# Optimization experiments

Hardware: AMD Instinct MI355X
Metric: run time of the kernel (lower is better)

The kernel has to match this reference:

```python
import jax, jax.numpy as jnp
import numpy as np

N_SP = 1024          # number of superpixels per image (max index + 1)
FEATURE_DIM = 256
HIDDEN_DIM = 128
OUTPUT_DIM = 64
TEMPERATURE = 0.1
B, H, W = 4, 256, 256


def setup_inputs() -> dict:
    key = jax.random.key(0)
    ks = jax.random.split(key, 12)
    features = jax.random.normal(ks[0], (B, FEATURE_DIM, H, W), dtype=jnp.float32)
    superpixel_indices = jax.random.randint(ks[1], (B, H, W), 0, N_SP, dtype=jnp.int32)
    s = 0.02
    return {
        "features": features,
        "superpixel_indices": superpixel_indices,
        "W1": jax.random.normal(ks[2], (HIDDEN_DIM, FEATURE_DIM), jnp.float32) * s,
        "b1": jnp.zeros((HIDDEN_DIM,), jnp.float32),
        "W2": jax.random.normal(ks[3], (HIDDEN_DIM, HIDDEN_DIM), jnp.float32) * s,
        "b2": jnp.zeros((HIDDEN_DIM,), jnp.float32),
        "Wp1": jax.random.normal(ks[4], (OUTPUT_DIM, HIDDEN_DIM), jnp.float32) * s,
        "bp1": jnp.zeros((OUTPUT_DIM,), jnp.float32),
        "Wp2": jax.random.normal(ks[5], (OUTPUT_DIM, HIDDEN_DIM), jnp.float32) * s,
        "bp2": jnp.zeros((OUTPUT_DIM,), jnp.float32),
    }


def _aggregate(feat, idx):
    # feat: [C,H,W], idx: [H,W] -> scatter-mean into [N_SP, C]
    C = feat.shape[0]
    feat_flat = feat.reshape(C, -1).T           # [HW, C]
    idx_flat = idx.reshape(-1)
    seg_sum = jax.ops.segment_sum(feat_flat, idx_flat, num_segments=N_SP)
    counts = jax.ops.segment_sum(jnp.ones_like(idx_flat, dtype=feat.dtype), idx_flat,
                                 num_segments=N_SP)[:, None]  # [N_SP,1]
    sp_feat = jnp.where(counts > 0, seg_sum / jnp.maximum(counts, 1.0), 0.0)
    return sp_feat


def _adjacency(idx):
    # idx: [H,W] int -> symmetric normalized adjacency [N_SP, N_SP]
    s1 = jnp.concatenate([idx[:, :-1].reshape(-1), idx[:-1, :].reshape(-1)])
    s2 = jnp.concatenate([idx[:, 1:].reshape(-1), idx[1:, :].reshape(-1)])
    diff = (s1 != s2).astype(jnp.float32)
    adj = jnp.zeros((N_SP, N_SP), jnp.float32).at[s1, s2].add(diff)
    adj = ((adj + adj.T) > 0).astype(jnp.float32) + jnp.eye(N_SP, dtype=jnp.float32)
    deg = jnp.sqrt(adj.sum(axis=1))
    adj = adj / (deg[:, None] * deg[None, :])
    return adj


def _infonce(z1, z2):
    z1 = z1 / jnp.linalg.norm(z1, axis=1, keepdims=True)
    z2 = z2 / jnp.linalg.norm(z2, axis=1, keepdims=True)
    sim = (z1 @ z2.T) / TEMPERATURE            # [N,N]
    loss = -jnp.diagonal(sim) + jax.scipy.special.logsumexp(sim, axis=1)
    return loss.mean()


def reference(features, superpixel_indices, W1, b1, W2, b2, Wp1, bp1, Wp2, bp2):
    def per_image(feat, idx):
        sp_feat = _aggregate(feat, idx)        # [N_SP, C]
        adj = _adjacency(idx)                  # [N_SP, N_SP]
        x = adj @ sp_feat                      # graph conv
        h = jax.nn.relu(x @ W1.T + b1)         # encoder (dropout = identity, eval)
        h = jax.nn.relu(h @ W2.T + b2)
        z1 = h @ Wp1.T + bp1
        z2 = h @ Wp2.T + bp2
        return _infonce(z1, z2)
    losses = jax.vmap(per_image)(features, superpixel_indices)
    return losses.mean()
```

## Files before the change

kernel.cpp:

```cpp
#include <hip/hip_runtime.h>
#include <math.h>

#define NB 4
#define NC 256
#define NPIX 65536
#define NSP 1024
#define OUTD 64

typedef short bfrag_t __attribute__((ext_vector_type(8)));
typedef float cfrag_t __attribute__((ext_vector_type(4)));
typedef float f32x2 __attribute__((ext_vector_type(2)));

__device__ __forceinline__ unsigned short f2bf(float f) {
    union { float f; unsigned u; } v; v.f = f;
    unsigned r = (v.u + 0x7FFFu + ((v.u >> 16) & 1u)) >> 16;
    return (unsigned short)r;
}
__device__ __forceinline__ float bf2f(unsigned short h) {
    union { unsigned u; float f; } v; v.u = ((unsigned)h) << 16;
    return v.f;
}

__global__ __launch_bounds__(256) void hist_kernel(const int* __restrict__ idx,
                                                   unsigned* __restrict__ counts_u) {
    __shared__ unsigned cnt[NSP];
    int b = blockIdx.y;
    int tid = threadIdx.x;
    for (int s = tid; s < NSP; s += 256) cnt[s] = 0u;
    __syncthreads();
    const int4* idx4 = (const int4*)(idx + b * NPIX + blockIdx.x * 1024);
    int4 s4 = idx4[tid];
    atomicAdd(&cnt[s4.x], 1u);
    atomicAdd(&cnt[s4.y], 1u);
    atomicAdd(&cnt[s4.z], 1u);
    atomicAdd(&cnt[s4.w], 1u);
    __syncthreads();
    for (int s = tid; s < NSP; s += 256)
        if (cnt[s]) atomicAdd(&counts_u[b * NSP + s], cnt[s]);
}

__global__ __launch_bounds__(256) void scan_kernel(const unsigned* __restrict__ counts_u,
                                                   unsigned* __restrict__ offsets,
                                                   unsigned* __restrict__ cursor) {
    int b = blockIdx.x;
    int tid = threadIdx.x;
    __shared__ unsigned v[256];
    unsigned c0 = counts_u[b * NSP + tid * 4 + 0];
    unsigned c1 = counts_u[b * NSP + tid * 4 + 1];
    unsigned c2 = counts_u[b * NSP + tid * 4 + 2];
    unsigned c3 = counts_u[b * NSP + tid * 4 + 3];
    v[tid] = c0 + c1 + c2 + c3;
    __syncthreads();
    for (int off = 1; off < 256; off <<= 1) {
        unsigned t = (tid >= off) ? v[tid - off] : 0u;
        __syncthreads();
        v[tid] += t;
        __syncthreads();
    }
    unsigned base = tid ? v[tid - 1] : 0u;
    unsigned o0 = base, o1 = base + c0, o2 = base + c0 + c1, o3 = base + c0 + c1 + c2;
    offsets[b * (NSP + 1) + tid * 4 + 0] = o0;
    offsets[b * (NSP + 1) + tid * 4 + 1] = o1;
    offsets[b * (NSP + 1) + tid * 4 + 2] = o2;
    offsets[b * (NSP + 1) + tid * 4 + 3] = o3;
    cursor[b * NSP + tid * 4 + 0] = o0;
    cursor[b * NSP + tid * 4 + 1] = o1;
    cursor[b * NSP + tid * 4 + 2] = o2;
    cursor[b * NSP + tid * 4 + 3] = o3;
    if (tid == 255) offsets[b * (NSP + 1) + NSP] = v[255];
}

__global__ __launch_bounds__(256) void rank_kernel(const int* __restrict__ idx,
                                                   unsigned* __restrict__ cursor,
                                                   int* __restrict__ rank) {
    __shared__ unsigned lcnt[NSP];
    __shared__ unsigned base[NSP];
    int b = blockIdx.y;
    int tid = threadIdx.x;
    for (int s = tid; s < NSP; s += 256) lcnt[s] = 0u;
    __syncthreads();
    const int4* idx4 = (const int4*)(idx + b * NPIX + blockIdx.x * 1024);
    int4 s4 = idx4[tid];
    unsigned r0 = atomicAdd(&lcnt[s4.x], 1u);
    unsigned r1 = atomicAdd(&lcnt[s4.y], 1u);
    unsigned r2 = atomicAdd(&lcnt[s4.z], 1u);
    unsigned r3 = atomicAdd(&lcnt[s4.w], 1u);
    __syncthreads();
    for (int s = tid; s < NSP; s += 256) {
        unsigned c = lcnt[s];
        base[s] = c ? atomicAdd(&cursor[b * NSP + s], c) : 0u;
    }
    __syncthreads();
    int p = b * NPIX + blockIdx.x * 1024 + tid * 4;
    rank[p + 0] = (int)(base[s4.x] + r0);
    rank[p + 1] = (int)(base[s4.y] + r1);
    rank[p + 2] = (int)(base[s4.z] + r2);
    rank[p + 3] = (int)(base[s4.w] + r3);
}

__global__ __launch_bounds__(256) void transpose_kernel(const float* __restrict__ feat,
                                                        const int* __restrict__ rank,
                                                        unsigned char* __restrict__ featP) {
    __shared__ unsigned short tile[64 * 260];
    __shared__ int rk[64];
    int b = blockIdx.y;
    int p0 = blockIdx.x * 64;
    int tid = threadIdx.x;
    if (tid < 64) rk[tid] = rank[b * NPIX + p0 + tid];
    int cg = tid >> 4;
    int x4 = tid & 15;
    #pragma unroll
    for (int pass = 0; pass < 16; ++pass) {
        int c = pass * 16 + cg;
        float4 v = *(const float4*)&feat[((size_t)(b * NC + c)) * NPIX + p0 + x4 * 4];
        tile[(x4 * 4 + 0) * 260 + c] = f2bf(v.x);
        tile[(x4 * 4 + 1) * 260 + c] = f2bf(v.y);
        tile[(x4 * 4 + 2) * 260 + c] = f2bf(v.z);
        tile[(x4 * 4 + 3) * 260 + c] = f2bf(v.w);
    }
    __syncthreads();
    int c4 = tid & 63;
    int r0 = tid >> 6;
    #pragma unroll
    for (int pass = 0; pass < 16; ++pass) {
        int row = pass * 4 + r0;
        ushort4 w = *(const ushort4*)&tile[row * 260 + c4 * 4];
        float f0 = bf2f(w.x), f1 = bf2f(w.y), f2 = bf2f(w.z), f3 = bf2f(w.w);
        int lo = __builtin_amdgcn_cvt_pk_fp8_f32(f0, f1, 0, false);
        int pk = __builtin_amdgcn_cvt_pk_fp8_f32(f2, f3, lo, true);
        *(unsigned*)&featP[((size_t)b * NPIX + rk[row]) * NC + c4 * 4] = (unsigned)pk;
    }
}

__global__ __launch_bounds__(256) void segsum_kernel(const unsigned char* __restrict__ featP,
                                                     const unsigned* __restrict__ offsets,
                                                     const float* __restrict__ deg_inv,
                                                     float* __restrict__ spf) {
    __shared__ float red[4][256];
    int b = blockIdx.y, s = blockIdx.x;
    int tid = threadIdx.x;
    int w = tid >> 6, lane = tid & 63;
    unsigned j0 = offsets[b * (NSP + 1) + s];
    unsigned j1 = offsets[b * (NSP + 1) + s + 1];
    const unsigned* base = (const unsigned*)(featP + (size_t)b * NPIX * NC);
    float a0 = 0.f, a1 = 0.f, a2 = 0.f, a3 = 0.f;
    for (unsigned j = j0 + w; j < j1; j += 4) {
        unsigned u = base[(size_t)j * 64 + lane];
        f32x2 lo = __builtin_amdgcn_cvt_pk_f32_fp8(u, false);
        f32x2 hi = __builtin_amdgcn_cvt_pk_f32_fp8(u, true);
        a0 += lo.x; a1 += lo.y; a2 += hi.x; a3 += hi.y;
    }
    *(float4*)&red[w][lane * 4] = (float4){a0, a1, a2, a3};
    __syncthreads();
    int c = tid;
    float sum = red[0][c] + red[1][c] + red[2][c] + red[3][c];
    unsigned cnt = j1 - j0;
    float scale = cnt ? deg_inv[b * NSP + s] / (float)cnt : 0.f;
    spf[((size_t)b * NSP + s) * NC + c] = sum * scale;
}

__global__ __launch_bounds__(256) void spft_kernel(const float* __restrict__ spf,
                                                   unsigned short* __restrict__ spfT) {
    __shared__ unsigned short t[64 * 68];
    int b = blockIdx.z;
    int s0 = blockIdx.x * 64, c0 = blockIdx.y * 64;
    int tid = threadIdx.x;
    int sl = tid >> 4, c4 = tid & 15;
    #pragma unroll
    for (int it = 0; it < 4; ++it) {
        int s = it * 16 + sl;
        float4 v = *(const float4*)&spf[((size_t)b * NSP + s0 + s) * NC + c0 + c4 * 4];
        t[(c4 * 4 + 0) * 68 + s] = f2bf(v.x);
        t[(c4 * 4 + 1) * 68 + s] = f2bf(v.y);
        t[(c4 * 4 + 2) * 68 + s] = f2bf(v.z);
        t[(c4 * 4 + 3) * 68 + s] = f2bf(v.w);
    }
    __syncthreads();
    int cl = tid >> 4, s4 = tid & 15;
    #pragma unroll
    for (int it = 0; it < 4; ++it) {
        int c = it * 16 + cl;
        ushort4 w = *(const ushort4*)&t[c * 68 + s4 * 4];
        *(ushort4*)&spfT[((size_t)b * NC + c0 + c) * NSP + s0 + s4 * 4] = w;
    }
}

__global__ __launch_bounds__(256) void adj_kernel(const int* __restrict__ idx,
                                                  unsigned short* __restrict__ adj) {
    const int PAIRS = 65280;
    const int PERB = 2 * PAIRS + NSP;
    int i = blockIdx.x * 256 + threadIdx.x;
    if (i >= NB * PERB) return;
    int b = i / PERB;
    int r = i % PERB;
    unsigned short* A = adj + (size_t)b * NSP * NSP;
    const int* id = idx + b * NPIX;
    if (r >= 2 * PAIRS) {
        int s = r - 2 * PAIRS;
        A[s * NSP + s] = 0x3F80;
        return;
    }
    int p1, p2;
    if (r < PAIRS) {
        int row = r / 255, col = r % 255;
        p1 = row * 256 + col; p2 = p1 + 1;
    } else {
        int rv = r - PAIRS;
        p1 = rv; p2 = rv + 256;
    }
    int s1 = id[p1], s2 = id[p2];
    if (s1 != s2) {
        A[s1 * NSP + s2] = 0x3F80;
        A[s2 * NSP + s1] = 0x3F80;
    }
}

__global__ __launch_bounds__(256) void deg_kernel(const unsigned short* __restrict__ adj,
                                                  float* __restrict__ deg_inv) {
    int row = blockIdx.x;
    int tid = threadIdx.x;
    const unsigned* a2 = (const unsigned*)(adj + (size_t)row * NSP);
    unsigned u0 = a2[tid], u1 = a2[tid + 256];
    float s = (float)((u0 & 0xFFFFu) != 0) + (float)((u0 >> 16) != 0)
            + (float)((u1 & 0xFFFFu) != 0) + (float)((u1 >> 16) != 0);
    for (int off = 32; off > 0; off >>= 1) s += __shfl_down(s, off, 64);
    __shared__ float wsum[4];
    if ((tid & 63) == 0) wsum[tid >> 6] = s;
    __syncthreads();
    if (tid == 0) deg_inv[row] = 1.0f / sqrtf(wsum[0] + wsum[1] + wsum[2] + wsum[3]);
}

__global__ __launch_bounds__(256) void conv_kernel(const unsigned short* __restrict__ adjb,
                                                   const unsigned short* __restrict__ spfT,
                                                   const float* __restrict__ deg_inv,
                                                   float* __restrict__ x) {
    __shared__ __align__(16) unsigned short Al[64 * 72];
    __shared__ __align__(16) unsigned short Bl[64 * 72];
    int b = blockIdx.z;
    int i0 = blockIdx.y * 64, c0 = blockIdx.x * 64;
    int tid = threadIdx.x;
    int wave = tid >> 6, lane = tid & 63;
    int wm = wave >> 1, wn = wave & 1;
    const unsigned short* A = adjb + (size_t)b * NSP * NSP;
    const unsigned short* Bt = spfT + (size_t)b * NC * NSP;
    cfrag_t acc[2][2] = {{{0.f, 0.f, 0.f, 0.f}, {0.f, 0.f, 0.f, 0.f}},
                         {{0.f, 0.f, 0.f, 0.f}, {0.f, 0.f, 0.f, 0.f}}};
    int sr2 = tid >> 3, sc2 = tid & 7;
    int q = lane >> 4, m = lane & 15;
    for (int kt = 0; kt < 16; ++kt) {
        int k0 = kt * 64;
        __syncthreads();
        *(uint4*)&Al[sr2 * 72 + sc2 * 8] =
            *(const uint4*)&A[(size_t)(i0 + sr2) * NSP + k0 + sc2 * 8];
        *(uint4*)&Al[(sr2 + 32) * 72 + sc2 * 8] =
            *(const uint4*)&A[(size_t)(i0 + sr2 + 32) * NSP + k0 + sc2 * 8];
        *(uint4*)&Bl[sr2 * 72 + sc2 * 8] =
            *(const uint4*)&Bt[(size_t)(c0 + sr2) * NSP + k0 + sc2 * 8];
        *(uint4*)&Bl[(sr2 + 32) * 72 + sc2 * 8] =
            *(const uint4*)&Bt[(size_t)(c0 + sr2 + 32) * NSP + k0 + sc2 * 8];
        __syncthreads();
        #pragma unroll
        for (int ks = 0; ks < 2; ++ks) {
            int kk = ks * 32 + q * 8;
            bfrag_t a0 = *(const bfrag_t*)&Al[(wm * 32 + m) * 72 + kk];
            bfrag_t a1 = *(const bfrag_t*)&Al[(wm * 32 + 16 + m) * 72 + kk];
            bfrag_t b0 = *(const bfrag_t*)&Bl[(wn * 32 + m) * 72 + kk];
            bfrag_t b1 = *(const bfrag_t*)&Bl[(wn * 32 + 16 + m) * 72 + kk];
            acc[0][0] = __builtin_amdgcn_mfma_f32_16x16x32_bf16(a0, b0, acc[0][0], 0, 0, 0);
            acc[0][1] = __builtin_amdgcn_mfma_f32_16x16x32_bf16(a0, b1, acc[0][1], 0, 0, 0);
            acc[1][0] = __builtin_amdgcn_mfma_f32_16x16x32_bf16(a1, b0, acc[1][0], 0, 0, 0);
            acc[1][1] = __builtin_amdgcn_mfma_f32_16x16x32_bf16(a1, b1, acc[1][1], 0, 0, 0);
        }
    }
    int col = lane & 15, rbase = (lane >> 4) * 4;
    #pragma unroll
    for (int mi = 0; mi < 2; ++mi) {
        #pragma unroll
        for (int reg = 0; reg < 4; ++reg) {
            int gi = i0 + wm * 32 + mi * 16 + rbase + reg;
            float di = deg_inv[b * NSP + gi];
            #pragma unroll
            for (int ni = 0; ni < 2; ++ni) {
                int gc = c0 + wn * 32 + ni * 16 + col;
                x[((size_t)b * NSP + gi) * NC + gc] = acc[mi][ni][reg] * di;
            }
        }
    }
}

__global__ __launch_bounds__(256) void encoder_kernel(
    const float* __restrict__ x,
    const float* __restrict__ W1, const float* __restrict__ b1,
    const float* __restrict__ W2, const float* __restrict__ b2,
    const float* __restrict__ Wp1, const float* __restrict__ bp1,
    const float* __restrict__ Wp2, const float* __restrict__ bp2,
    float* __restrict__ z1g, float* __restrict__ z2g) {
    __shared__ float xs[16 * 260];
    __shared__ float h1s[16 * 132];
    __shared__ float h2s[16 * 132];
    __shared__ float red1[16 * 17], red2[16 * 17];
    __shared__ float inv1[16], inv2[16];
    int blk = blockIdx.x;
    int b = blk >> 6;
    int r0 = (blk & 63) * 16;
    int tid = threadIdx.x;
    for (int it = 0; it < 4; ++it) {
        int fl = it * 256 + tid;
        int row = fl >> 6, c4 = fl & 63;
        float4 v = *(const float4*)&x[((size_t)b * NSP + r0 + row) * NC + c4 * 4];
        *(float4*)&xs[row * 260 + c4 * 4] = v;
    }
    __syncthreads();
    int r = tid & 15, tc = tid >> 4;
    float acc[8] = {};
    for (int k4 = 0; k4 < 64; ++k4) {
        float4 xv = *(const float4*)&xs[r * 260 + k4 * 4];
        #pragma unroll
        for (int u = 0; u < 8; ++u) {
            int n = tc * 8 + u;
            float4 wv = *(const float4*)&W1[n * 256 + k4 * 4];
            acc[u] += xv.x * wv.x + xv.y * wv.y + xv.z * wv.z + xv.w * wv.w;
        }
    }
    #pragma unroll
    for (int u = 0; u < 8; ++u) {
        int n = tc * 8 + u;
        h1s[r * 132 + n] = fmaxf(acc[u] + b1[n], 0.f);
    }
    __syncthreads();
    float acc2[8] = {};
    for (int k4 = 0; k4 < 32; ++k4) {
        float4 hv = *(const float4*)&h1s[r * 132 + k4 * 4];
        #pragma unroll
        for (int u = 0; u < 8; ++u) {
            int n = tc * 8 + u;
            float4 wv = *(const float4*)&W2[n * 128 + k4 * 4];
            acc2[u] += hv.x * wv.x + hv.y * wv.y + hv.z * wv.z + hv.w * wv.w;
        }
    }
    #pragma unroll
    for (int u = 0; u < 8; ++u) {
        int n = tc * 8 + u;
        h2s[r * 132 + n] = fmaxf(acc2[u] + b2[n], 0.f);
    }
    __syncthreads();
    float az1[4] = {}, az2[4] = {};
    for (int k4 = 0; k4 < 32; ++k4) {
        float4 hv = *(const float4*)&h2s[r * 132 + k4 * 4];
        #pragma unroll
        for (int u = 0; u < 4; ++u) {
            int n = tc * 4 + u;
            float4 w1v = *(const float4*)&Wp1[n * 128 + k4 * 4];
            float4 w2v = *(const float4*)&Wp2[n * 128 + k4 * 4];
            az1[u] += hv.x * w1v.x + hv.y * w1v.y + hv.z * w1v.z + hv.w * w1v.w;
            az2[u] += hv.x * w2v.x + hv.y * w2v.y + hv.z * w2v.z + hv.w * w2v.w;
        }
    }
    float ss1 = 0.f, ss2 = 0.f;
    #pragma unroll
    for (int u = 0; u < 4; ++u) {
        int n = tc * 4 + u;
        az1[u] += bp1[n]; az2[u] += bp2[n];
        ss1 += az1[u] * az1[u];
        ss2 += az2[u] * az2[u];
    }
    red1[r * 17 + tc] = ss1;
    red2[r * 17 + tc] = ss2;
    __syncthreads();
    if (tid < 16) {
        float s1 = 0.f, s2 = 0.f;
        for (int t = 0; t < 16; ++t) { s1 += red1[tid * 17 + t]; s2 += red2[tid * 17 + t]; }
        inv1[tid] = 1.0f / sqrtf(s1);
        inv2[tid] = 1.0f / sqrtf(s2);
    }
    __syncthreads();
    float i1 = inv1[r], i2 = inv2[r];
    float4 o1 = {az1[0] * i1, az1[1] * i1, az1[2] * i1, az1[3] * i1};
    float4 o2 = {az2[0] * i2, az2[1] * i2, az2[2] * i2, az2[3] * i2};
    *(float4*)&z1g[((size_t)b * NSP + r0 + r) * OUTD + tc * 4] = o1;
    *(float4*)&z2g[((size_t)b * NSP + r0 + r) * OUTD + tc * 4] = o2;
}

__global__ __launch_bounds__(256) void infonce_kernel(const float* __restrict__ z1g,
                                                      const float* __restrict__ z2g,
                                                      float* __restrict__ row_loss) {
    __shared__ float z1s[16 * 68];
    __shared__ float z2s[16 * 68];
    __shared__ float reds[16 * 17];
    __shared__ float diag[16];
    int blk = blockIdx.x;
    int b = blk >> 6;
    int i0 = (blk & 63) * 16;
    int tid = threadIdx.x;
    int lrow = tid >> 4, lc4 = tid & 15;
    float4 v = *(const float4*)&z1g[((size_t)b * NSP + i0 + lrow) * OUTD + lc4 * 4];
    v.x *= 10.0f; v.y *= 10.0f; v.z *= 10.0f; v.w *= 10.0f;
    *(float4*)&z1s[lrow * 68 + lc4 * 4] = v;
    int ti = tid >> 4, tj = tid & 15;
    float lsum = 0.f;
    for (int jt = 0; jt < 64; ++jt) {
        __syncthreads();
        float4 w = *(const float4*)&z2g[((size_t)b * NSP + jt * 16 + lrow) * OUTD + lc4 * 4];
        *(float4*)&z2s[lrow * 68 + lc4 * 4] = w;
        __syncthreads();
        float dot = 0.f;
        #pragma unroll
        for (int k4 = 0; k4 < 16; ++k4) {
            float4 a = *(const float4*)&z1s[ti * 68 + k4 * 4];
            float4 bb = *(const float4*)&z2s[tj * 68 + k4 * 4];
            dot += a.x * bb.x + a.y * bb.y + a.z * bb.z + a.w * bb.w;
        }
        lsum += __expf(dot);
        if (jt * 16 + tj == i0 + ti) diag[ti] = dot;
    }
    reds[ti * 17 + tj] = lsum;
    __syncthreads();
    if (tid < 16) {
        float tot = 0.f;
        for (int t = 0; t < 16; ++t) tot += reds[tid * 17 + t];
        row_loss[b * NSP + i0 + tid] = -diag[tid] + __logf(tot);
    }
}

__global__ __launch_bounds__(256) void reduce_kernel(const float* __restrict__ row_loss,
                                                     float* __restrict__ out) {
    int tid = threadIdx.x;
    float s = 0.f;
    for (int i = tid; i < NB * NSP; i += 256) s += row_loss[i];
    for (int off = 32; off > 0; off >>= 1) s += __shfl_down(s, off, 64);
    __shared__ float wsum[4];
    if ((tid & 63) == 0) wsum[tid >> 6] = s;
    __syncthreads();
    if (tid == 0) out[0] = (wsum[0] + wsum[1] + wsum[2] + wsum[3]) * (1.0f / (NB * NSP));
}

extern "C" void kernel_launch(void* const* d_in, const int* in_sizes, int n_in,
                              void* d_out, int out_size, void* d_ws, size_t ws_size,
                              hipStream_t stream) {
    const float* feat = (const float*)d_in[0];
    const int* idx = (const int*)d_in[1];
    const float* W1 = (const float*)d_in[2];
    const float* b1 = (const float*)d_in[3];
    const float* W2 = (const float*)d_in[4];
    const float* b2 = (const float*)d_in[5];
    const float* Wp1 = (const float*)d_in[6];
    const float* bp1 = (const float*)d_in[7];
    const float* Wp2 = (const float*)d_in[8];
    const float* bp2 = (const float*)d_in[9];

    char* wsb = (char*)d_ws;
    size_t off = 0;
    auto alloc = [&](size_t bytes) -> void* {
        void* p = wsb + off;
        off += (bytes + 255) & ~(size_t)255;
        return p;
    };
    unsigned short* adjb  = (unsigned short*)alloc((size_t)NB * NSP * NSP * 2);
    float* deg_inv        = (float*)alloc((size_t)NB * NSP * 4);
    float* spf            = (float*)alloc((size_t)NB * NSP * NC * 4);
    unsigned short* spfT  = (unsigned short*)alloc((size_t)NB * NC * NSP * 2);
    float* x              = (float*)alloc((size_t)NB * NSP * NC * 4);
    float* z1g            = (float*)alloc((size_t)NB * NSP * OUTD * 4);
    float* z2g            = (float*)alloc((size_t)NB * NSP * OUTD * 4);
    float* row_loss       = (float*)alloc((size_t)NB * NSP * 4);
    unsigned* counts_u    = (unsigned*)alloc((size_t)NB * NSP * 4);
    unsigned* offsets     = (unsigned*)alloc((size_t)NB * (NSP + 1) * 4);
    unsigned* cursor      = (unsigned*)alloc((size_t)NB * NSP * 4);
    int* rank             = (int*)alloc((size_t)NB * NPIX * 4);
    unsigned char* featP  = (unsigned char*)alloc((size_t)NB * NPIX * NC);

    hipMemsetAsync(adjb, 0, (size_t)NB * NSP * NSP * 2, stream);
    hipMemsetAsync(counts_u, 0, (size_t)NB * NSP * 4, stream);

    hist_kernel<<<dim3(64, NB), 256, 0, stream>>>(idx, counts_u);
    scan_kernel<<<NB, 256, 0, stream>>>(counts_u, offsets, cursor);
    rank_kernel<<<dim3(64, NB), 256, 0, stream>>>(idx, cursor, rank);

    int total_adj = NB * (2 * 65280 + NSP);
    adj_kernel<<<(total_adj + 255) / 256, 256, 0, stream>>>(idx, adjb);
    deg_kernel<<<NB * NSP, 256, 0, stream>>>(adjb, deg_inv);

    transpose_kernel<<<dim3(NPIX / 64, NB), 256, 0, stream>>>(feat, rank, featP);
    segsum_kernel<<<dim3(NSP, NB), 256, 0, stream>>>(featP, offsets, deg_inv, spf);
    spft_kernel<<<dim3(NSP / 64, NC / 64, NB), 256, 0, stream>>>(spf, spfT);

    conv_kernel<<<dim3(NC / 64, NSP / 64, NB), 256, 0, stream>>>(adjb, spfT, deg_inv, x);
    encoder_kernel<<<NB * 64, 256, 0, stream>>>(x, W1, b1, W2, b2, Wp1, bp1, Wp2, bp2, z1g, z2g);
    infonce_kernel<<<NB * 64, 256, 0, stream>>>(z1g, z2g, row_loss);
    reduce_kernel<<<1, 256, 0, stream>>>(row_loss, (float*)d_out);
}
```

Baseline: 560.4 us.

## Replace sort-based segment sum with LDS atomic scatter-add per channel group

Drops the counting-sort pipeline (scan, rank, fp8 transposed copy, per-segment gather) and replaces it with a kernel where each block owns 4 channels of one image. The block streams all pixels and scatter-adds them into LDS float accumulators with atomics. The mean and degree scaling move into the spf transpose kernel. This removes the rank/featP global writes and several launches, and it also drops the fp8 quantization so sums are full fp32. The cost is heavy LDS atomic traffic, and only 256 blocks each read 4 full channel planes plus the index map.

```diff
diff --git a/kernel.cpp b/kernel.cpp
--- a/kernel.cpp
+++ b/kernel.cpp
@@ -9,16 +9,11 @@
 
 typedef short bfrag_t __attribute__((ext_vector_type(8)));
 typedef float cfrag_t __attribute__((ext_vector_type(4)));
-typedef float f32x2 __attribute__((ext_vector_type(2)));
 
 __device__ __forceinline__ unsigned short f2bf(float f) {
     union { float f; unsigned u; } v; v.f = f;
     unsigned r = (v.u + 0x7FFFu + ((v.u >> 16) & 1u)) >> 16;
     return (unsigned short)r;
-}
-__device__ __forceinline__ float bf2f(unsigned short h) {
-    union { unsigned u; float f; } v; v.u = ((unsigned)h) << 16;
-    return v.f;
 }
 
 __global__ __launch_bounds__(256) void hist_kernel(const int* __restrict__ idx,
@@ -39,127 +34,54 @@
         if (cnt[s]) atomicAdd(&counts_u[b * NSP + s], cnt[s]);
 }
 
-__global__ __launch_bounds__(256) void scan_kernel(const unsigned* __restrict__ counts_u,
-                                                   unsigned* __restrict__ offsets,
-                                                   unsigned* __restrict__ cursor) {
-    int b = blockIdx.x;
-    int tid = threadIdx.x;
-    __shared__ unsigned v[256];
-    unsigned c0 = counts_u[b * NSP + tid * 4 + 0];
-    unsigned c1 = counts_u[b * NSP + tid * 4 + 1];
-    unsigned c2 = counts_u[b * NSP + tid * 4 + 2];
-    unsigned c3 = counts_u[b * NSP + tid * 4 + 3];
-    v[tid] = c0 + c1 + c2 + c3;
-    __syncthreads();
-    for (int off = 1; off < 256; off <<= 1) {
-        unsigned t = (tid >= off) ? v[tid - off] : 0u;
-        __syncthreads();
-        v[tid] += t;
-        __syncthreads();
-    }
-    unsigned base = tid ? v[tid - 1] : 0u;
-    unsigned o0 = base, o1 = base + c0, o2 = base + c0 + c1, o3 = base + c0 + c1 + c2;
-    offsets[b * (NSP + 1) + tid * 4 + 0] = o0;
-    offsets[b * (NSP + 1) + tid * 4 + 1] = o1;
-    offsets[b * (NSP + 1) + tid * 4 + 2] = o2;
-    offsets[b * (NSP + 1) + tid * 4 + 3] = o3;
-    cursor[b * NSP + tid * 4 + 0] = o0;
-    cursor[b * NSP + tid * 4 + 1] = o1;
-    cursor[b * NSP + tid * 4 + 2] = o2;
-    cursor[b * NSP + tid * 4 + 3] = o3;
-    if (tid == 255) offsets[b * (NSP + 1) + NSP] = v[255];
-}
-
-__global__ __launch_bounds__(256) void rank_kernel(const int* __restrict__ idx,
-                                                   unsigned* __restrict__ cursor,
-                                                   int* __restrict__ rank) {
-    __shared__ unsigned lcnt[NSP];
-    __shared__ unsigned base[NSP];
+__global__ __launch_bounds__(256) void agg_kernel(const float* __restrict__ feat,
+                                                  const int* __restrict__ idx,
+                                                  float* __restrict__ spf) {
+    __shared__ float acc[4][NSP];
     int b = blockIdx.y;
-    int tid = threadIdx.x;
-    for (int s = tid; s < NSP; s += 256) lcnt[s] = 0u;
-    __syncthreads();
-    const int4* idx4 = (const int4*)(idx + b * NPIX + blockIdx.x * 1024);
-    int4 s4 = idx4[tid];
-    unsigned r0 = atomicAdd(&lcnt[s4.x], 1u);
-    unsigned r1 = atomicAdd(&lcnt[s4.y], 1u);
-    unsigned r2 = atomicAdd(&lcnt[s4.z], 1u);
-    unsigned r3 = atomicAdd(&lcnt[s4.w], 1u);
+    int c0 = blockIdx.x * 4;
+    int tid = threadIdx.x;
+    for (int i = tid; i < 4 * NSP; i += 256) ((float*)acc)[i] = 0.f;
+    __syncthreads();
+    const int4* idx4 = (const int4*)(idx + b * NPIX);
+    const float4* f0 = (const float4*)(feat + ((size_t)(b * NC + c0 + 0)) * NPIX);
+    const float4* f1 = (const float4*)(feat + ((size_t)(b * NC + c0 + 1)) * NPIX);
+    const float4* f2 = (const float4*)(feat + ((size_t)(b * NC + c0 + 2)) * NPIX);
+    const float4* f3 = (const float4*)(feat + ((size_t)(b * NC + c0 + 3)) * NPIX);
+    for (int it = 0; it < NPIX / 2048; ++it) {
+        int pa = it * 512 + tid;
+        int pb = pa + 256;
+        int4 sa = idx4[pa];
+        int4 sb = idx4[pb];
+        float4 a0 = f0[pa], a1 = f1[pa], a2 = f2[pa], a3 = f3[pa];
+        float4 b0 = f0[pb], b1 = f1[pb], b2 = f2[pb], b3 = f3[pb];
+        atomicAdd(&acc[0][sa.x], a0.x); atomicAdd(&acc[0][sa.y], a0.y);
+        atomicAdd(&acc[0][sa.z], a0.z); atomicAdd(&acc[0][sa.w], a0.w);
+        atomicAdd(&acc[1][sa.x], a1.x); atomicAdd(&acc[1][sa.y], a1.y);
+        atomicAdd(&acc[1][sa.z], a1.z); atomicAdd(&acc[1][sa.w], a1.w);
+        atomicAdd(&acc[2][sa.x], a2.x); atomicAdd(&acc[2][sa.y], a2.y);
+        atomicAdd(&acc[2][sa.z], a2.z); atomicAdd(&acc[2][sa.w], a2.w);
+        atomicAdd(&acc[3][sa.x], a3.x); atomicAdd(&acc[3][sa.y], a3.y);
+        atomicAdd(&acc[3][sa.z], a3.z); atomicAdd(&acc[3][sa.w], a3.w);
+        atomicAdd(&acc[0][sb.x], b0.x); atomicAdd(&acc[0][sb.y], b0.y);
+        atomicAdd(&acc[0][sb.z], b0.z); atomicAdd(&acc[0][sb.w], b0.w);
+        atomicAdd(&acc[1][sb.x], b1.x); atomicAdd(&acc[1][sb.y], b1.y);
+        atomicAdd(&acc[1][sb.z], b1.z); atomicAdd(&acc[1][sb.w], b1.w);
+        atomicAdd(&acc[2][sb.x], b2.x); atomicAdd(&acc[2][sb.y], b2.y);
+        atomicAdd(&acc[2][sb.z], b2.z); atomicAdd(&acc[2][sb.w], b2.w);
+        atomicAdd(&acc[3][sb.x], b3.x); atomicAdd(&acc[3][sb.y], b3.y);
+        atomicAdd(&acc[3][sb.z], b3.z); atomicAdd(&acc[3][sb.w], b3.w);
+    }
     __syncthreads();
     for (int s = tid; s < NSP; s += 256) {
-        unsigned c = lcnt[s];
-        base[s] = c ? atomicAdd(&cursor[b * NSP + s], c) : 0u;
-    }
-    __syncthreads();
-    int p = b * NPIX + blockIdx.x * 1024 + tid * 4;
-    rank[p + 0] = (int)(base[s4.x] + r0);
-    rank[p + 1] = (int)(base[s4.y] + r1);
-    rank[p + 2] = (int)(base[s4.z] + r2);
-    rank[p + 3] = (int)(base[s4.w] + r3);
-}
-
-__global__ __launch_bounds__(256) void transpose_kernel(const float* __restrict__ feat,
-                                                        const int* __restrict__ rank,
-                                                        unsigned char* __restrict__ featP) {
-    __shared__ unsigned short tile[64 * 260];
-    __shared__ int rk[64];
-    int b = blockIdx.y;
-    int p0 = blockIdx.x * 64;
-    int tid = threadIdx.x;
-    if (tid < 64) rk[tid] = rank[b * NPIX + p0 + tid];
-    int cg = tid >> 4;
-    int x4 = tid & 15;
-    #pragma unroll
-    for (int pass = 0; pass < 16; ++pass) {
-        int c = pass * 16 + cg;
-        float4 v = *(const float4*)&feat[((size_t)(b * NC + c)) * NPIX + p0 + x4 * 4];
-        tile[(x4 * 4 + 0) * 260 + c] = f2bf(v.x);
-        tile[(x4 * 4 + 1) * 260 + c] = f2bf(v.y);
-        tile[(x4 * 4 + 2) * 260 + c] = f2bf(v.z);
-        tile[(x4 * 4 + 3) * 260 + c] = f2bf(v.w);
-    }
-    __syncthreads();
-    int c4 = tid & 63;
-    int r0 = tid >> 6;
-    #pragma unroll
-    for (int pass = 0; pass < 16; ++pass) {
-        int row = pass * 4 + r0;
-        ushort4 w = *(const ushort4*)&tile[row * 260 + c4 * 4];
-        float f0 = bf2f(w.x), f1 = bf2f(w.y), f2 = bf2f(w.z), f3 = bf2f(w.w);
-        int lo = __builtin_amdgcn_cvt_pk_fp8_f32(f0, f1, 0, false);
-        int pk = __builtin_amdgcn_cvt_pk_fp8_f32(f2, f3, lo, true);
-        *(unsigned*)&featP[((size_t)b * NPIX + rk[row]) * NC + c4 * 4] = (unsigned)pk;
-    }
-}
-
-__global__ __launch_bounds__(256) void segsum_kernel(const unsigned char* __restrict__ featP,
-                                                     const unsigned* __restrict__ offsets,
-                                                     const float* __restrict__ deg_inv,
-                                                     float* __restrict__ spf) {
-    __shared__ float red[4][256];
-    int b = blockIdx.y, s = blockIdx.x;
-    int tid = threadIdx.x;
-    int w = tid >> 6, lane = tid & 63;
-    unsigned j0 = offsets[b * (NSP + 1) + s];
-    unsigned j1 = offsets[b * (NSP + 1) + s + 1];
-    const unsigned* base = (const unsigned*)(featP + (size_t)b * NPIX * NC);
-    float a0 = 0.f, a1 = 0.f, a2 = 0.f, a3 = 0.f;
-    for (unsigned j = j0 + w; j < j1; j += 4) {
-        unsigned u = base[(size_t)j * 64 + lane];
-        f32x2 lo = __builtin_amdgcn_cvt_pk_f32_fp8(u, false);
-        f32x2 hi = __builtin_amdgcn_cvt_pk_f32_fp8(u, true);
-        a0 += lo.x; a1 += lo.y; a2 += hi.x; a3 += hi.y;
-    }
-    *(float4*)&red[w][lane * 4] = (float4){a0, a1, a2, a3};
-    __syncthreads();
-    int c = tid;
-    float sum = red[0][c] + red[1][c] + red[2][c] + red[3][c];
-    unsigned cnt = j1 - j0;
-    float scale = cnt ? deg_inv[b * NSP + s] / (float)cnt : 0.f;
-    spf[((size_t)b * NSP + s) * NC + c] = sum * scale;
+        float4 o = {acc[0][s], acc[1][s], acc[2][s], acc[3][s]};
+        *(float4*)&spf[((size_t)b * NSP + s) * NC + c0] = o;
+    }
 }
 
 __global__ __launch_bounds__(256) void spft_kernel(const float* __restrict__ spf,
+                                                   const unsigned* __restrict__ counts_u,
+                                                   const float* __restrict__ deg_inv,
                                                    unsigned short* __restrict__ spfT) {
     __shared__ unsigned short t[64 * 68];
     int b = blockIdx.z;
@@ -169,11 +91,13 @@
     #pragma unroll
     for (int it = 0; it < 4; ++it) {
         int s = it * 16 + sl;
+        unsigned cnt = counts_u[b * NSP + s0 + s];
+        float scl = cnt ? deg_inv[b * NSP + s0 + s] / (float)cnt : 0.f;
         float4 v = *(const float4*)&spf[((size_t)b * NSP + s0 + s) * NC + c0 + c4 * 4];
-        t[(c4 * 4 + 0) * 68 + s] = f2bf(v.x);
-        t[(c4 * 4 + 1) * 68 + s] = f2bf(v.y);
-        t[(c4 * 4 + 2) * 68 + s] = f2bf(v.z);
-        t[(c4 * 4 + 3) * 68 + s] = f2bf(v.w);
+        t[(c4 * 4 + 0) * 68 + s] = f2bf(v.x * scl);
+        t[(c4 * 4 + 1) * 68 + s] = f2bf(v.y * scl);
+        t[(c4 * 4 + 2) * 68 + s] = f2bf(v.z * scl);
+        t[(c4 * 4 + 3) * 68 + s] = f2bf(v.w * scl);
     }
     __syncthreads();
     int cl = tid >> 4, s4 = tid & 15;
@@ -464,25 +388,18 @@
     float* z2g            = (float*)alloc((size_t)NB * NSP * OUTD * 4);
     float* row_loss       = (float*)alloc((size_t)NB * NSP * 4);
     unsigned* counts_u    = (unsigned*)alloc((size_t)NB * NSP * 4);
-    unsigned* offsets     = (unsigned*)alloc((size_t)NB * (NSP + 1) * 4);
-    unsigned* cursor      = (unsigned*)alloc((size_t)NB * NSP * 4);
-    int* rank             = (int*)alloc((size_t)NB * NPIX * 4);
-    unsigned char* featP  = (unsigned char*)alloc((size_t)NB * NPIX * NC);
 
     hipMemsetAsync(adjb, 0, (size_t)NB * NSP * NSP * 2, stream);
     hipMemsetAsync(counts_u, 0, (size_t)NB * NSP * 4, stream);
 
     hist_kernel<<<dim3(64, NB), 256, 0, stream>>>(idx, counts_u);
-    scan_kernel<<<NB, 256, 0, stream>>>(counts_u, offsets, cursor);
-    rank_kernel<<<dim3(64, NB), 256, 0, stream>>>(idx, cursor, rank);
 
     int total_adj = NB * (2 * 65280 + NSP);
     adj_kernel<<<(total_adj + 255) / 256, 256, 0, stream>>>(idx, adjb);
     deg_kernel<<<NB * NSP, 256, 0, stream>>>(adjb, deg_inv);
 
-    transpose_kernel<<<dim3(NPIX / 64, NB), 256, 0, stream>>>(feat, rank, featP);
-    segsum_kernel<<<dim3(NSP, NB), 256, 0, stream>>>(featP, offsets, deg_inv, spf);
-    spft_kernel<<<dim3(NSP / 64, NC / 64, NB), 256, 0, stream>>>(spf, spfT);
+    agg_kernel<<<dim3(NC / 4, NB), 256, 0, stream>>>(feat, idx, spf);
+    spft_kernel<<<dim3(NSP / 64, NC / 64, NB), 256, 0, stream>>>(spf, counts_u, deg_inv, spfT);
 
     conv_kernel<<<dim3(NC / 64, NSP / 64, NB), 256, 0, stream>>>(adjb, spfT, deg_inv, x);
     encoder_kernel<<<NB * 64, 256, 0, stream>>>(x, W1, b1, W2, b2, Wp1, bp1, Wp2, bp2, z1g, z2g);
```

After: 760.5 us. 1.36x slower.
